# Kernel tuning notes

Hardware: AMD Instinct MI355X
Metric: run time of the kernel (lower is better)

The kernel has to match this reference:

```python
import jax, jax.numpy as jnp
import numpy as np

B, S, D = 8, 2048, 2048
E, R, K = 8, 16, 2
NUM_TASKS, NUM_MODES = 4, 2
ALPHA = 16.0


def setup_inputs() -> dict:
    key = jax.random.key(0)
    k1, k2, k3, k4 = jax.random.split(key, 4)
    hidden_states = jax.random.normal(k1, (B, S, D), dtype=jnp.float32)
    gate_w = jax.random.normal(k2, (E, D), dtype=jnp.float32) * 0.01  # nn.init.normal_(std=0.01)
    # Soft-prior biases: fill(-1.0), strong prior 3.0 / 2.0 at configured (task, expert) / (mode, expert)
    tb = -np.ones((NUM_TASKS, E), dtype=np.float32)
    mb = -np.ones((NUM_MODES, E), dtype=np.float32)
    for e in range(E):
        tb[e % NUM_TASKS, e] = 3.0
        mb[e % NUM_MODES, e] = 2.0
    # LoRA params; lora_B is zero-init in torch but we use small random values for a nontrivial baseline
    lora_A = jax.random.normal(k3, (E, R, D), dtype=jnp.float32) * (1.0 / np.sqrt(D))
    lora_B = jax.random.normal(k4, (E, D, R), dtype=jnp.float32) * 0.02
    return {
        "hidden_states": hidden_states,
        "gate_w": gate_w,
        "task_bias": jnp.asarray(tb),
        "mode_bias": jnp.asarray(mb),
        "lora_A": lora_A,
        "lora_B": lora_B,
        "task_id": 1,
        "mode_id": 1,
    }


def reference(hidden_states, gate_w, task_bias, mode_bias, lora_A, lora_B, task_id, mode_id):
    scaling = ALPHA / R
    # Router: score = dynamic_gate(mean_pool(x)) + task_bias[t] + mode_bias[m]
    x_pooled = hidden_states.mean(axis=1)                       # [B, D]
    logits = x_pooled @ gate_w.T + task_bias[task_id] + mode_bias[mode_id]  # [B, E]
    top_v, top_i = jax.lax.top_k(logits, K)                     # [B, K]
    weights = jax.nn.softmax(top_v, axis=-1)                    # [B, K]
    # per-sample, per-expert combine weight: sum of top-k weights routed to that expert
    one_hot = jax.nn.one_hot(top_i, E, dtype=weights.dtype)     # [B, K, E]
    sw = jnp.einsum('bke,bk->be', one_hot, weights)             # [B, E]
    # LoRA experts: (x @ A_e^T) @ B_e^T * scaling, weighted-summed per sample
    mid = jnp.einsum('bsd,erd->besr', hidden_states, lora_A)    # [B, E, S, R] (small: R=16)
    out = jnp.einsum('be,besr,edr->bsd', sw, mid, lora_B) * scaling  # [B, S, D]
    return out
```

## Files before the change

### kernel.cpp

```cpp
#include <hip/hip_runtime.h>
#include <stdint.h>

typedef __attribute__((ext_vector_type(8))) short bf16x8;
typedef __attribute__((ext_vector_type(4))) float f32x4;
typedef unsigned short ushort_t;

#define B_ 8
#define S_ 2048
#define D_ 2048
#define E_ 8
#define J_ 128

static __device__ __forceinline__ unsigned short f2bf(float f) {
  union { float f; uint32_t u; } v; v.f = f;
  uint32_t u = v.u;
  return (unsigned short)((u + 0x7FFFu + ((u >> 16) & 1u)) >> 16);
}
static __device__ __forceinline__ float bf2f(ushort_t h) {
  union { uint32_t u; float f; } v; v.u = ((uint32_t)h) << 16;
  return v.f;
}

#define GLL16(gsrc, ldst)                                                        \
  __builtin_amdgcn_global_load_lds(                                              \
      (const __attribute__((address_space(1))) void*)(gsrc),                     \
      (__attribute__((address_space(3))) void*)(ldst), 16, 0, 0)

__global__ void k_prep(const float* __restrict__ lA, const float* __restrict__ lB,
                       ushort_t* __restrict__ Ag, ushort_t* __restrict__ Bg) {
  int gid = blockIdx.x * blockDim.x + threadIdx.x;
  int stride = gridDim.x * blockDim.x;
  for (int o = gid; o < 32 * 128 * 8 * 8; o += stride) {
    int wi = o & 7, ch = o >> 3;
    int kt = ch >> 10, i = ch & 1023;
    int j = i >> 3, c = i & 7;
    int d = kt * 64 + (((c ^ j) & 7) << 3) + wi;
    Ag[o] = f2bf(lA[j * D_ + d]);
  }
  for (int o4 = gid; o4 < (D_ * J_) / 4; o4 += stride) {
    int j4 = o4 & 31, dd = o4 >> 5;
    int e = j4 >> 2, r0 = (j4 & 3) * 4;
    float4 v = *(const float4*)(lB + ((size_t)e * D_ + dd) * 16 + r0);
    uint2 pk;
    pk.x = (uint32_t)f2bf(v.x) | ((uint32_t)f2bf(v.y) << 16);
    pk.y = (uint32_t)f2bf(v.z) | ((uint32_t)f2bf(v.w) << 16);
    ((uint2*)Bg)[o4] = pk;
  }
}

__global__ __launch_bounds__(256) void k_mid(const float* __restrict__ x,
    const ushort_t* __restrict__ Ag, const float* __restrict__ gw,
    ushort_t* __restrict__ midb, float* __restrict__ lpart) {
  __shared__ float Xs[2][2048];
  __shared__ ushort_t Ab[2][8192];
  __shared__ float tmpP[2][4][64];
  const int tid = threadIdx.x;
  const int w = tid >> 6, lane = tid & 63;
  const int lm = lane & 15, g = lane >> 4;
  const int b = blockIdx.y, s0 = blockIdx.x * 32;
  const int row16 = (w & 1) * 16, jbase = (w >> 1) * 64;
  const float* xb = x + ((size_t)(b * S_ + s0)) * D_;

  f32x4 acc[4] = {};
  float lp0 = 0.f, lp1 = 0.f;
  float gwc0 = 0.f, gwc1 = 0.f;
  const float* gw0 = gw + (size_t)(2 * w) * D_;
  const float* gw1 = gw + (size_t)(2 * w + 1) * D_;

  auto stageX = [&](int buf, int kt) {
    const int d0 = kt * 64;
#pragma unroll
    for (int c = 0; c < 2; ++c) {
      int i = c * 256 + w * 64 + lane;
      int row = i >> 4, ch = i & 15;
      const float* src = xb + (size_t)row * D_ + d0 + ((ch ^ (row & 7)) << 2);
      GLL16(src, &Xs[buf][(c * 256 + w * 64) * 4]);
    }
  };
  auto stageA = [&](int buf, int kt) {
#pragma unroll
    for (int c = 0; c < 4; ++c) {
      const ushort_t* src = Ag + (size_t)kt * 8192 + (size_t)(c * 256 + w * 64 + lane) * 8;
      GLL16(src, &Ab[buf][(c * 256 + w * 64) * 8]);
    }
  };

  stageX(0, 0); stageA(0, 0);
  __syncthreads();

  for (int t = 0; t < 32; ++t) {
    const int cb = t & 1;
    if (t + 1 < 32) { stageX(cb ^ 1, t + 1); stageA(cb ^ 1, t + 1); }
    if (t > 0) {
      const int pb = cb ^ 1;
      float cs = tmpP[pb][0][lane] + tmpP[pb][1][lane] +
                 tmpP[pb][2][lane] + tmpP[pb][3][lane];
      lp0 += cs * gwc0;
      lp1 += cs * gwc1;
    }
    gwc0 = gw0[t * 64 + lane];
    gwc1 = gw1[t * 64 + lane];
    const int r = row16 + lm;
#pragma unroll
    for (int ks = 0; ks < 2; ++ks) {
      const int c0 = ks * 8 + g * 2;
      float4 v0 = *(const float4*)&Xs[cb][r * 64 + ((c0 ^ (r & 7)) << 2)];
      float4 v1 = *(const float4*)&Xs[cb][r * 64 + (((c0 + 1) ^ (r & 7)) << 2)];
      bf16x8 xf;
      xf[0] = (short)f2bf(v0.x); xf[1] = (short)f2bf(v0.y);
      xf[2] = (short)f2bf(v0.z); xf[3] = (short)f2bf(v0.w);
      xf[4] = (short)f2bf(v1.x); xf[5] = (short)f2bf(v1.y);
      xf[6] = (short)f2bf(v1.z); xf[7] = (short)f2bf(v1.w);
#pragma unroll
      for (int nn = 0; nn < 4; ++nn) {
        int jr = jbase + nn * 16 + lm;
        bf16x8 af = *(const bf16x8*)&Ab[cb][jr * 64 + (((ks * 4 + g) ^ (jr & 7)) << 3)];
        acc[nn] = __builtin_amdgcn_mfma_f32_16x16x32_bf16(af, xf, acc[nn], 0, 0, 0);
      }
    }
    {
      float s = 0.f;
#pragma unroll
      for (int i = 0; i < 8; ++i) {
        int rr = w * 8 + i;
        s += Xs[cb][rr * 64 + (((lane >> 2) ^ (rr & 7)) << 2) + (lane & 3)];
      }
      tmpP[cb][w][lane] = s;
    }
    __syncthreads();
  }
  {
    float cs = tmpP[1][0][lane] + tmpP[1][1][lane] +
               tmpP[1][2][lane] + tmpP[1][3][lane];
    lp0 += cs * gwc0;
    lp1 += cs * gwc1;
  }
#pragma unroll
  for (int off = 32; off; off >>= 1) {
    lp0 += __shfl_xor(lp0, off);
    lp1 += __shfl_xor(lp1, off);
  }
  if (lane == 0) {
    float* lp = lpart + ((size_t)(b * 64 + blockIdx.x)) * 8;
    lp[2 * w] = lp0;
    lp[2 * w + 1] = lp1;
  }
  ushort_t* mp = midb + ((size_t)(b * S_ + s0 + row16 + lm)) * J_ + jbase;
#pragma unroll
  for (int nn = 0; nn < 4; ++nn) {
    uint2 pk;
    pk.x = (uint32_t)f2bf(acc[nn][0]) | ((uint32_t)f2bf(acc[nn][1]) << 16);
    pk.y = (uint32_t)f2bf(acc[nn][2]) | ((uint32_t)f2bf(acc[nn][3]) << 16);
    *(uint2*)&mp[nn * 16 + g * 4] = pk;
  }
}

__global__ void k_router(const float* __restrict__ lpart,
                         const float* __restrict__ tb, const float* __restrict__ mb,
                         const int* __restrict__ task_p, const int* __restrict__ mode_p,
                         float* __restrict__ rinfo) {
  __shared__ float lg[64];
  const int t = threadIdx.x;
  const int b = t >> 3, e = t & 7;
  float s = 0.f;
  for (int k = 0; k < 64; ++k) s += lpart[((size_t)(b * 64 + k)) * 8 + e];
  lg[t] = s * (1.f / (float)S_) + tb[task_p[0] * E_ + e] + mb[mode_p[0] * E_ + e];
  __syncthreads();
  if (t < B_) {
    float v[8];
#pragma unroll
    for (int e2 = 0; e2 < 8; ++e2) v[e2] = lg[t * 8 + e2];
    int i1 = 0;
#pragma unroll
    for (int e2 = 1; e2 < 8; ++e2) if (v[e2] > v[i1]) i1 = e2;
    int i2 = (i1 == 0) ? 1 : 0;
#pragma unroll
    for (int e2 = 0; e2 < 8; ++e2) if (e2 != i1 && v[e2] > v[i2]) i2 = e2;
    float ex = __expf(v[i2] - v[i1]);
    float w1 = 1.f / (1.f + ex), w2 = ex * w1;
    float4 r;
    r.x = (float)i1; r.y = (float)i2; r.z = w1; r.w = w2;
    ((float4*)rinfo)[t] = r;
  }
}

__global__ __launch_bounds__(256) void k_comb(const ushort_t* __restrict__ midb,
    const float* __restrict__ rinfo, const ushort_t* __restrict__ Bg,
    float* __restrict__ out) {
  __shared__ ushort_t Bt[128][40];
  const int n = blockIdx.x, m = blockIdx.y, b = blockIdx.z;
  const int tid = threadIdx.x, w = tid >> 6, lane = tid & 63;
  const int lm = lane & 15, g = lane >> 4;

  const float4 ri = ((const float4*)rinfo)[b];
  const int i1 = (int)ri.x, i2 = (int)ri.y;
  const float w1 = ri.z, w2 = ri.w;

#pragma unroll
  for (int c = 0; c < 2; ++c) {
    int ci = c * 256 + tid;
    int d = ci >> 2, sub = ci & 3;
    int e = (sub & 2) ? i2 : i1;
    float sc = (sub & 2) ? w2 : w1;
    bf16x8 bv = *(const bf16x8*)(Bg + ((size_t)(n * 128 + d)) * J_ + e * 16 + (sub & 1) * 8);
    bf16x8 bw;
#pragma unroll
    for (int i = 0; i < 8; ++i) bw[i] = (short)f2bf(bf2f((ushort_t)bv[i]) * sc);
    *(bf16x8*)&Bt[d][sub * 8] = bw;
  }

  const int srow = m * 64 + w * 16 + lm;
  const int jw = (g < 2) ? (i1 * 16 + g * 8) : (i2 * 16 + (g - 2) * 8);
  bf16x8 pf = *(const bf16x8*)&midb[((size_t)(b * S_ + srow)) * J_ + jw];
  __syncthreads();

  f32x4 acc[8] = {};
#pragma unroll
  for (int nn = 0; nn < 8; ++nn) {
    bf16x8 af = *(const bf16x8*)&Bt[nn * 16 + lm][g * 8];
    acc[nn] = __builtin_amdgcn_mfma_f32_16x16x32_bf16(af, pf, acc[nn], 0, 0, 0);
  }

  float* op = out + ((size_t)(b * S_ + srow)) * D_ + n * 128;
#pragma unroll
  for (int nn = 0; nn < 8; ++nn)
    *(f32x4*)&op[nn * 16 + g * 4] = acc[nn];
}

extern "C" void kernel_launch(void* const* d_in, const int* in_sizes, int n_in,
                              void* d_out, int out_size, void* d_ws, size_t ws_size,
                              hipStream_t stream) {
  const float* x    = (const float*)d_in[0];
  const float* gw   = (const float*)d_in[1];
  const float* tb   = (const float*)d_in[2];
  const float* mb   = (const float*)d_in[3];
  const float* lA   = (const float*)d_in[4];
  const float* lB   = (const float*)d_in[5];
  const int* task_p = (const int*)d_in[6];
  const int* mode_p = (const int*)d_in[7];
  float* out = (float*)d_out;
  char* ws = (char*)d_ws;
  ushort_t* midb  = (ushort_t*)ws;
  ushort_t* Ag    = (ushort_t*)(ws + 4194304);
  ushort_t* Bg    = (ushort_t*)(ws + 4718592);
  float* lpart    = (float*)(ws + 5242880);
  float* rinfo    = (float*)(ws + 5259264);

  hipLaunchKernelGGL(k_prep, dim3(256), dim3(256), 0, stream, lA, lB, Ag, Bg);
  hipLaunchKernelGGL(k_mid, dim3(64, 8), dim3(256), 0, stream, x, Ag, gw, midb, lpart);
  hipLaunchKernelGGL(k_router, dim3(1), dim3(64), 0, stream,
                     lpart, tb, mb, task_p, mode_p, rinfo);
  hipLaunchKernelGGL(k_comb, dim3(16, 32, 8), dim3(256), 0, stream, midb, rinfo, Bg, out);
}
```

Baseline: 93.99 us.

## Triple-buffer X tiles with vmcnt barriers and defer gate dot to epilogue

The k_mid main loop goes from double to triple buffering of the X tile, and __syncthreads is replaced by explicit s_waitcnt vmcnt(N) plus s_barrier, so two X loads stay in flight while the current tile computes. The per-iteration gate-weight dot product is removed from the loop. Column sums are now saved to a shared pool buffer and multiplied by gate_w once in an epilogue. This aims to hide global-load latency and shorten the inner loop, at the cost of more LDS per block, which may reduce occupancy.

```diff
diff --git a/kernel.cpp b/kernel.cpp
--- a/kernel.cpp
+++ b/kernel.cpp
@@ -25,6 +25,9 @@
   __builtin_amdgcn_global_load_lds(                                              \
       (const __attribute__((address_space(1))) void*)(gsrc),                     \
       (__attribute__((address_space(3))) void*)(ldst), 16, 0, 0)
+
+#define VMBAR(N)                                                                 \
+  asm volatile("s_waitcnt vmcnt(" #N ") lgkmcnt(0)\n\ts_barrier" ::: "memory")
 
 __global__ void k_prep(const float* __restrict__ lA, const float* __restrict__ lB,
                        ushort_t* __restrict__ Ag, ushort_t* __restrict__ Bg) {
@@ -51,8 +54,9 @@
 __global__ __launch_bounds__(256) void k_mid(const float* __restrict__ x,
     const ushort_t* __restrict__ Ag, const float* __restrict__ gw,
     ushort_t* __restrict__ midb, float* __restrict__ lpart) {
-  __shared__ float Xs[2][2048];
+  __shared__ float Xs[3][2048];
   __shared__ ushort_t Ab[2][8192];
+  __shared__ float poolL[2048];
   __shared__ float tmpP[2][4][64];
   const int tid = threadIdx.x;
   const int w = tid >> 6, lane = tid & 63;
@@ -62,10 +66,6 @@
   const float* xb = x + ((size_t)(b * S_ + s0)) * D_;
 
   f32x4 acc[4] = {};
-  float lp0 = 0.f, lp1 = 0.f;
-  float gwc0 = 0.f, gwc1 = 0.f;
-  const float* gw0 = gw + (size_t)(2 * w) * D_;
-  const float* gw1 = gw + (size_t)(2 * w + 1) * D_;
 
   auto stageX = [&](int buf, int kt) {
     const int d0 = kt * 64;
@@ -84,28 +84,13 @@
       GLL16(src, &Ab[buf][(c * 256 + w * 64) * 8]);
     }
   };
-
-  stageX(0, 0); stageA(0, 0);
-  __syncthreads();
-
-  for (int t = 0; t < 32; ++t) {
-    const int cb = t & 1;
-    if (t + 1 < 32) { stageX(cb ^ 1, t + 1); stageA(cb ^ 1, t + 1); }
-    if (t > 0) {
-      const int pb = cb ^ 1;
-      float cs = tmpP[pb][0][lane] + tmpP[pb][1][lane] +
-                 tmpP[pb][2][lane] + tmpP[pb][3][lane];
-      lp0 += cs * gwc0;
-      lp1 += cs * gwc1;
-    }
-    gwc0 = gw0[t * 64 + lane];
-    gwc1 = gw1[t * 64 + lane];
+  auto computeTile = [&](int t, int xcb, int acb) {
     const int r = row16 + lm;
 #pragma unroll
     for (int ks = 0; ks < 2; ++ks) {
       const int c0 = ks * 8 + g * 2;
-      float4 v0 = *(const float4*)&Xs[cb][r * 64 + ((c0 ^ (r & 7)) << 2)];
-      float4 v1 = *(const float4*)&Xs[cb][r * 64 + (((c0 + 1) ^ (r & 7)) << 2)];
+      float4 v0 = *(const float4*)&Xs[xcb][r * 64 + ((c0 ^ (r & 7)) << 2)];
+      float4 v1 = *(const float4*)&Xs[xcb][r * 64 + (((c0 + 1) ^ (r & 7)) << 2)];
       bf16x8 xf;
       xf[0] = (short)f2bf(v0.x); xf[1] = (short)f2bf(v0.y);
       xf[2] = (short)f2bf(v0.z); xf[3] = (short)f2bf(v0.w);
@@ -114,37 +99,52 @@
 #pragma unroll
       for (int nn = 0; nn < 4; ++nn) {
         int jr = jbase + nn * 16 + lm;
-        bf16x8 af = *(const bf16x8*)&Ab[cb][jr * 64 + (((ks * 4 + g) ^ (jr & 7)) << 3)];
+        bf16x8 af = *(const bf16x8*)&Ab[acb][jr * 64 + (((ks * 4 + g) ^ (jr & 7)) << 3)];
         acc[nn] = __builtin_amdgcn_mfma_f32_16x16x32_bf16(af, xf, acc[nn], 0, 0, 0);
       }
     }
-    {
-      float s = 0.f;
-#pragma unroll
-      for (int i = 0; i < 8; ++i) {
-        int rr = w * 8 + i;
-        s += Xs[cb][rr * 64 + (((lane >> 2) ^ (rr & 7)) << 2) + (lane & 3)];
-      }
-      tmpP[cb][w][lane] = s;
-    }
-    __syncthreads();
-  }
-  {
-    float cs = tmpP[1][0][lane] + tmpP[1][1][lane] +
-               tmpP[1][2][lane] + tmpP[1][3][lane];
-    lp0 += cs * gwc0;
-    lp1 += cs * gwc1;
-  }
-#pragma unroll
-  for (int off = 32; off; off >>= 1) {
-    lp0 += __shfl_xor(lp0, off);
-    lp1 += __shfl_xor(lp1, off);
-  }
-  if (lane == 0) {
-    float* lp = lpart + ((size_t)(b * 64 + blockIdx.x)) * 8;
-    lp[2 * w] = lp0;
-    lp[2 * w + 1] = lp1;
-  }
+    float s = 0.f;
+#pragma unroll
+    for (int i = 0; i < 8; ++i) {
+      int rr = w * 8 + i;
+      s += Xs[xcb][rr * 64 + (((lane >> 2) ^ (rr & 7)) << 2) + (lane & 3)];
+    }
+    tmpP[t & 1][w][lane] = s;
+  };
+  auto foldTile = [&](int tau) {
+    if (w == (tau & 3)) {
+      float cs = tmpP[tau & 1][0][lane] + tmpP[tau & 1][1][lane] +
+                 tmpP[tau & 1][2][lane] + tmpP[tau & 1][3][lane];
+      poolL[tau * 64 + lane] = cs;
+    }
+  };
+
+  stageA(0, 0);
+  __builtin_amdgcn_sched_barrier(0);
+  stageX(0, 0);
+  __builtin_amdgcn_sched_barrier(0);
+  stageX(1, 1);
+  __builtin_amdgcn_sched_barrier(0);
+
+  int xcb = 0, xsb = 2;
+  for (int t = 0; t < 31; ++t) {
+    VMBAR(2);
+    __builtin_amdgcn_sched_barrier(0);
+    const int acb = t & 1;
+    stageA(acb ^ 1, t + 1);
+    __builtin_amdgcn_sched_barrier(0);
+    if (t + 2 < 32) stageX(xsb, t + 2);
+    __builtin_amdgcn_sched_barrier(0);
+    if (t > 0) foldTile(t - 1);
+    computeTile(t, xcb, acb);
+    xcb = (xcb == 2) ? 0 : xcb + 1;
+    xsb = (xsb == 2) ? 0 : xsb + 1;
+  }
+  VMBAR(0);
+  __builtin_amdgcn_sched_barrier(0);
+  foldTile(30);
+  computeTile(31, xcb, 1);
+
   ushort_t* mp = midb + ((size_t)(b * S_ + s0 + row16 + lm)) * J_ + jbase;
 #pragma unroll
   for (int nn = 0; nn < 4; ++nn) {
@@ -152,6 +152,30 @@
     pk.x = (uint32_t)f2bf(acc[nn][0]) | ((uint32_t)f2bf(acc[nn][1]) << 16);
     pk.y = (uint32_t)f2bf(acc[nn][2]) | ((uint32_t)f2bf(acc[nn][3]) << 16);
     *(uint2*)&mp[nn * 16 + g * 4] = pk;
+  }
+
+  __syncthreads();
+  foldTile(31);
+  __syncthreads();
+
+  float lp[8] = {0.f, 0.f, 0.f, 0.f, 0.f, 0.f, 0.f, 0.f};
+#pragma unroll
+  for (int k = 0; k < 8; ++k) {
+    float pv = poolL[k * 256 + tid];
+#pragma unroll
+    for (int e = 0; e < 8; ++e) lp[e] += pv * gw[(size_t)e * D_ + k * 256 + tid];
+  }
+#pragma unroll
+  for (int e = 0; e < 8; ++e) {
+    float v = lp[e];
+    v += __shfl_xor(v, 32); v += __shfl_xor(v, 16); v += __shfl_xor(v, 8);
+    v += __shfl_xor(v, 4);  v += __shfl_xor(v, 2);  v += __shfl_xor(v, 1);
+    if (lane == 0) tmpP[0][w][e] = v;
+  }
+  __syncthreads();
+  if (tid < 8) {
+    float s = tmpP[0][0][tid] + tmpP[0][1][tid] + tmpP[0][2][tid] + tmpP[0][3][tid];
+    lpart[((size_t)(b * 64 + blockIdx.x)) * 8 + tid] = s;
   }
 }
 
```

Result: faster. 88.78 us (-5.5%).
